# Kernel optimization log

Hardware: AMD Instinct MI355X
Metric: run time of the kernel (lower is better)

## Reference

```python
import jax, jax.numpy as jnp
import numpy as np

B, NQ, NKV, D = 2, 2048, 4096, 1024
H, DH = 16, 64            # qk_channels = v_channels = 1024 -> 16 heads x 64
HID = 2 * int(4.0 * D)    # GEGLU produces 8192 -> split into 2x4096
EPS = 1e-6


def layernorm(x, scale, bias):
    mu = jnp.mean(x, axis=-1, keepdims=True)
    var = jnp.mean(jnp.square(x - mu), axis=-1, keepdims=True)
    return (x - mu) * jax.lax.rsqrt(var + EPS) * scale + bias


def setup_inputs() -> dict:
    key = jax.random.key(0)
    ks = jax.random.split(key, 12)
    s = 0.02
    return {
        "inputs_q": jax.random.normal(ks[0], (B, NQ, D), jnp.float32),
        "inputs_kv": jax.random.normal(ks[1], (B, NKV, D), jnp.float32),
        "ln_q_scale": jnp.ones((D,), jnp.float32),
        "ln_q_bias": jnp.zeros((D,), jnp.float32),
        "ln_kv_scale": jnp.ones((D,), jnp.float32),
        "ln_kv_bias": jnp.zeros((D,), jnp.float32),
        "Wq": s * jax.random.normal(ks[2], (D, H, DH), jnp.float32),
        "bq": jnp.zeros((H, DH), jnp.float32),
        "Wk": s * jax.random.normal(ks[3], (D, H, DH), jnp.float32),
        "bk": jnp.zeros((H, DH), jnp.float32),
        "Wv": s * jax.random.normal(ks[4], (D, H, DH), jnp.float32),
        "bv": jnp.zeros((H, DH), jnp.float32),
        "Wo": s * jax.random.normal(ks[5], (H, DH, D), jnp.float32),
        "bo": jnp.zeros((D,), jnp.float32),
        "ln2_scale": jnp.ones((D,), jnp.float32),
        "ln2_bias": jnp.zeros((D,), jnp.float32),
        "W1": s * jax.random.normal(ks[6], (D, HID), jnp.float32),
        "b1": jnp.zeros((HID,), jnp.float32),
        "W2": s * jax.random.normal(ks[7], (HID // 2, D), jnp.float32),
        "b2": jnp.zeros((D,), jnp.float32),
    }


def reference(inputs_q, inputs_kv, ln_q_scale, ln_q_bias, ln_kv_scale, ln_kv_bias,
              Wq, bq, Wk, bk, Wv, bv, Wo, bo, ln2_scale, ln2_bias, W1, b1, W2, b2):
    ln_q = layernorm(inputs_q, ln_q_scale, ln_q_bias)
    ln_kv = layernorm(inputs_kv, ln_kv_scale, ln_kv_bias)
    # multi-head projections: DenseGeneral to (H, DH)
    q = jnp.einsum('bqd,dhe->bqhe', ln_q, Wq) + bq
    k = jnp.einsum('bkd,dhe->bkhe', ln_kv, Wk) + bk
    v = jnp.einsum('bkd,dhe->bkhe', ln_kv, Wv) + bv
    # scaled dot-product attention (full score matrix, as in source)
    attn = jnp.einsum('bqhd,bkhd->bhqk', q, k) / np.sqrt(DH).astype(np.float32)
    attn = jax.nn.softmax(attn, axis=-1)
    o = jnp.einsum('bhqk,bkhd->bqhd', attn, v)
    # output projection contracting (H, DH)
    x = jnp.einsum('bqhd,hdo->bqo', o, Wo) + bo
    x = x + inputs_q  # query residual
    # GEGLU MLP
    h = layernorm(x, ln2_scale, ln2_bias)
    h = jnp.dot(h, W1) + b1
    a, g = jnp.split(h, 2, axis=-1)
    h = a * jax.nn.gelu(g)  # approximate (tanh) gelu, flax default
    y = jnp.dot(h, W2) + b2
    return x + y
```

## Files before the change

kernel.cpp:

```cpp
#include <hip/hip_runtime.h>

typedef unsigned short u16;
typedef unsigned int u32;
typedef float f32x4 __attribute__((ext_vector_type(4)));
typedef float f32x16 __attribute__((ext_vector_type(16)));
typedef __bf16 bf16x8 __attribute__((ext_vector_type(8)));
typedef short s16x8 __attribute__((ext_vector_type(8)));
typedef short s16x4 __attribute__((ext_vector_type(4)));
typedef u32 u32x4 __attribute__((ext_vector_type(4)));

#define MFMA16(a, b, c) __builtin_amdgcn_mfma_f32_16x16x32_bf16((a), (b), (c), 0, 0, 0)
#define MFMA32(a, b, c) __builtin_amdgcn_mfma_f32_32x32x16_bf16((a), (b), (c), 0, 0, 0)

typedef const __attribute__((address_space(1))) void* gas1_t;
typedef __attribute__((address_space(3))) void* las3_t;
#define GLDS16(g, l) __builtin_amdgcn_global_load_lds((gas1_t)(g), (las3_t)(l), 16, 0, 0)

static __device__ __forceinline__ u16 f2bf(float f) {
  u32 u = __builtin_bit_cast(u32, f);
  u += 0x7FFFu + ((u >> 16) & 1u);
  return (u16)(u >> 16);
}
static __device__ __forceinline__ float bf2f(u16 h) {
  return __builtin_bit_cast(float, (u32)h << 16);
}
static __device__ __forceinline__ u32 cvtpk(float lo, float hi) {
  u32 r;
  asm("v_cvt_pk_bf16_f32 %0, %1, %2" : "=v"(r) : "v"(lo), "v"(hi));
  return r;
}

__global__ __launch_bounds__(256) void transp_cvt(const float* __restrict__ in,
                                                  u16* __restrict__ out, int K, int N,
                                                  float scale) {
  __shared__ u16 t[64][72];
  int k0 = blockIdx.x * 64, n0 = blockIdx.y * 64;
#pragma unroll
  for (int i = 0; i < 16; ++i) {
    int idx = threadIdx.x + i * 256;
    int r = idx >> 6, c = idx & 63;
    t[r][c] = f2bf(in[(size_t)(k0 + r) * N + n0 + c] * scale);
  }
  __syncthreads();
#pragma unroll
  for (int i = 0; i < 16; ++i) {
    int idx = threadIdx.x + i * 256;
    int r = idx >> 6, c = idx & 63;
    out[(size_t)(n0 + r) * K + k0 + c] = t[c][r];
  }
}

__global__ __launch_bounds__(256) void ln_bf16(const float* __restrict__ x,
                                               const float* __restrict__ sc,
                                               const float* __restrict__ bi,
                                               u16* __restrict__ out) {
  int row = blockIdx.x;
  int tid = threadIdx.x;
  float4 v = ((const float4*)(x + (size_t)row * 1024))[tid];
  float s = v.x + v.y + v.z + v.w;
  float s2 = v.x * v.x + v.y * v.y + v.z * v.z + v.w * v.w;
  for (int m = 1; m < 64; m <<= 1) {
    s += __shfl_xor(s, m);
    s2 += __shfl_xor(s2, m);
  }
  __shared__ float rs[4], rs2[4];
  int wave = tid >> 6, lane = tid & 63;
  if (lane == 0) { rs[wave] = s; rs2[wave] = s2; }
  __syncthreads();
  s = rs[0] + rs[1] + rs[2] + rs[3];
  s2 = rs2[0] + rs2[1] + rs2[2] + rs2[3];
  float mu = s * (1.0f / 1024.0f);
  float var = s2 * (1.0f / 1024.0f) - mu * mu;
  float inv = rsqrtf(var + 1e-6f);
  float4 scv = ((const float4*)sc)[tid];
  float4 biv = ((const float4*)bi)[tid];
  s16x4 o;
  o[0] = (short)f2bf((v.x - mu) * inv * scv.x + biv.x);
  o[1] = (short)f2bf((v.y - mu) * inv * scv.y + biv.y);
  o[2] = (short)f2bf((v.z - mu) * inv * scv.z + biv.z);
  o[3] = (short)f2bf((v.w - mu) * inv * scv.w + biv.w);
  *(s16x4*)(out + (size_t)row * 1024 + tid * 4) = o;
}

template <int MODE>
__global__ __launch_bounds__(256) void gemm_nt(const u16* __restrict__ A,
                                               const u16* __restrict__ Bt,
                                               const float* __restrict__ bias,
                                               const float* __restrict__ resid,
                                               void* __restrict__ Cout,
                                               int M, int N, int K, float bias_scale) {
  __shared__ u16 As[128 * 64];
  __shared__ u16 Bs[128 * 64];
  const int m0 = blockIdx.x * 128, n0 = blockIdx.y * 128;
  const int tid = threadIdx.x;
  const int lane = tid & 63, wave = tid >> 6;
  const int wm = (wave >> 1) * 64, wn = (wave & 1) * 64;
  const int lr = lane & 15, hi4 = lane >> 4;
  f32x4 acc[4][4] = {};
  for (int k0 = 0; k0 < K; k0 += 64) {
#pragma unroll
    for (int i = 0; i < 4; ++i) {
      int s = i * 256 + tid;
      int r = s >> 3, slot = s & 7;
      int gslot = slot ^ (r & 7);
      int ldst = (i * 256 + wave * 64) * 8;
      GLDS16(A + (size_t)(m0 + r) * K + k0 + gslot * 8, &As[ldst]);
      GLDS16(Bt + (size_t)(n0 + r) * K + k0 + gslot * 8, &Bs[ldst]);
    }
    __syncthreads();
#pragma unroll
    for (int ks = 0; ks < 2; ++ks) {
      const int sl = ((ks * 4 + hi4) ^ (lr & 7)) * 8;
      bf16x8 af[4], bfr[4];
#pragma unroll
      for (int t = 0; t < 4; ++t) {
        af[t] = __builtin_bit_cast(bf16x8, *(const s16x8*)&As[(wm + t * 16 + lr) * 64 + sl]);
        bfr[t] = __builtin_bit_cast(bf16x8, *(const s16x8*)&Bs[(wn + t * 16 + lr) * 64 + sl]);
      }
#pragma unroll
      for (int mt = 0; mt < 4; ++mt)
#pragma unroll
        for (int nt = 0; nt < 4; ++nt)
          acc[mt][nt] = MFMA16(af[mt], bfr[nt], acc[mt][nt]);
    }
    __syncthreads();
  }
#pragma unroll
  for (int mt = 0; mt < 4; ++mt) {
#pragma unroll
    for (int nt = 0; nt < 4; ++nt) {
      const int ncol = n0 + wn + nt * 16 + lr;
      const float bv = bias[ncol] * bias_scale;
      const int mbase = m0 + wm + mt * 16 + hi4 * 4;
#pragma unroll
      for (int r = 0; r < 4; ++r) {
        const int m = mbase + r;
        const float val = acc[mt][nt][r] + bv;
        if constexpr (MODE == 0) {
          ((u16*)Cout)[(size_t)m * N + ncol] = f2bf(val);
        } else if constexpr (MODE == 1) {
          size_t vidx = ((size_t)((m >> 12) * 1024 + ncol) << 12) | (size_t)(m & 4095);
          ((u16*)Cout)[vidx] = f2bf(val);
        } else {
          ((float*)Cout)[(size_t)m * N + ncol] = val + resid[(size_t)m * N + ncol];
        }
      }
    }
  }
}

__global__ __launch_bounds__(256, 2) void flash_attn(const u16* __restrict__ Qg,
                                                     const u16* __restrict__ Kg,
                                                     const u16* __restrict__ Vt,
                                                     u16* __restrict__ Og) {
  __shared__ u16 Ks[2][64 * 64];
  __shared__ u16 Vs[2][64 * 64];
  const int id = blockIdx.x;
  const int bh = (id & 7) * 4 + ((id >> 3) & 3);
  const int qb = id >> 5;
  const int b = bh >> 4, h = bh & 15;
  const int q0 = qb * 128;
  const int tid = threadIdx.x;
  const int lane = tid & 63, wave = tid >> 6;
  const int lq = lane & 31, hi = lane >> 5;
  const u16* Kbase = Kg + (size_t)(b * 4096) * 1024 + h * 64;
  const u16* Vbase = Vt + (size_t)((b * 16 + h) * 64) * 4096;
  bf16x8 qf[4];
  const size_t qrow = (size_t)(b * 2048 + q0 + wave * 32 + lq);
#pragma unroll
  for (int dc = 0; dc < 4; ++dc)
    qf[dc] = __builtin_bit_cast(bf16x8, *(const s16x8*)&Qg[qrow * 1024 + h * 64 + dc * 16 + hi * 8]);

  f32x16 oacc0 = {}, oacc1 = {};
  float lrun = 0.0f;

  auto stage = [&](int buf, int tile) {
    const int kv0 = tile * 64;
#pragma unroll
    for (int i = 0; i < 2; ++i) {
      int s = i * 256 + tid;
      int r = s >> 3;
      int inb = ((s & 7) * 16) ^ ((r & 7) << 4);
      GLDS16(Kbase + (size_t)(kv0 + r) * 1024 + (inb >> 1), &Ks[buf][(i * 256 + wave * 64) * 8]);
    }
#pragma unroll
    for (int i = 0; i < 2; ++i) {
      int s = i * 256 + tid;
      int r = s >> 3;
      int inb = ((s & 7) * 16) ^ ((r & 7) << 4);
      GLDS16(Vbase + (size_t)r * 4096 + kv0 + (inb >> 1), &Vs[buf][(i * 256 + wave * 64) * 8]);
    }
  };

  stage(0, 0);
  __syncthreads();
  int cur = 0;
  for (int t = 0; t < 64; ++t) {
    if (t < 63) stage(cur ^ 1, t + 1);
    f32x16 sA = {}, sB = {};
#pragma unroll
    for (int dc = 0; dc < 4; ++dc) {
      int row = lq;
      int inb = (dc * 32 + hi * 16) ^ ((row & 7) << 4);
      bf16x8 kf = __builtin_bit_cast(bf16x8, *(const s16x8*)&Ks[cur][row * 64 + (inb >> 1)]);
      sA = MFMA32(kf, qf[dc], sA);
    }
#pragma unroll
    for (int dc = 0; dc < 4; ++dc) {
      int row = 32 + lq;
      int inb = (dc * 32 + hi * 16) ^ ((row & 7) << 4);
      bf16x8 kf = __builtin_bit_cast(bf16x8, *(const s16x8*)&Ks[cur][row * 64 + (inb >> 1)]);
      sB = MFMA32(kf, qf[dc], sB);
    }
    float ts = 0.0f;
#pragma unroll
    for (int i = 0; i < 16; ++i) {
      float p = __builtin_amdgcn_exp2f(sA[i]);
      sA[i] = p;
      ts += p;
    }
#pragma unroll
    for (int i = 0; i < 16; ++i) {
      float p = __builtin_amdgcn_exp2f(sB[i]);
      sB[i] = p;
      ts += p;
    }
    ts += __shfl_xor(ts, 32);
    lrun += ts;
    u32 wa[8], wb[8];
#pragma unroll
    for (int i = 0; i < 8; ++i) wa[i] = cvtpk(sA[2 * i], sA[2 * i + 1]);
#pragma unroll
    for (int i = 0; i < 8; ++i) wb[i] = cvtpk(sB[2 * i], sB[2 * i + 1]);
    u32 a0 = wa[0], c0 = wa[2];
    asm("v_permlane32_swap_b32 %0, %1" : "+v"(a0), "+v"(c0));
    u32 a1 = wa[1], c1 = wa[3];
    asm("v_permlane32_swap_b32 %0, %1" : "+v"(a1), "+v"(c1));
    u32 a2 = wa[4], c2 = wa[6];
    asm("v_permlane32_swap_b32 %0, %1" : "+v"(a2), "+v"(c2));
    u32 a3 = wa[5], c3 = wa[7];
    asm("v_permlane32_swap_b32 %0, %1" : "+v"(a3), "+v"(c3));
    u32 e0 = wb[0], g0 = wb[2];
    asm("v_permlane32_swap_b32 %0, %1" : "+v"(e0), "+v"(g0));
    u32 e1 = wb[1], g1 = wb[3];
    asm("v_permlane32_swap_b32 %0, %1" : "+v"(e1), "+v"(g1));
    u32 e2 = wb[4], g2 = wb[6];
    asm("v_permlane32_swap_b32 %0, %1" : "+v"(e2), "+v"(g2));
    u32 e3 = wb[5], g3 = wb[7];
    asm("v_permlane32_swap_b32 %0, %1" : "+v"(e3), "+v"(g3));
    u32x4 t00 = {a0, a1, c0, c1};
    u32x4 t01 = {a2, a3, c2, c3};
    u32x4 t10 = {e0, e1, g0, g1};
    u32x4 t11 = {e2, e3, g2, g3};
    bf16x8 p00 = __builtin_bit_cast(bf16x8, t00);
    bf16x8 p01 = __builtin_bit_cast(bf16x8, t01);
    bf16x8 p10 = __builtin_bit_cast(bf16x8, t10);
    bf16x8 p11 = __builtin_bit_cast(bf16x8, t11);
#pragma unroll
    for (int st = 0; st < 2; ++st) {
      bf16x8 pc0 = st ? p10 : p00;
      bf16x8 pc1 = st ? p11 : p01;
#pragma unroll
      for (int c = 0; c < 2; ++c) {
        bf16x8 pf = c ? pc1 : pc0;
        {
          int row = lq;
          int inb = (st * 64 + c * 32 + hi * 16) ^ ((row & 7) << 4);
          bf16x8 vf = __builtin_bit_cast(bf16x8, *(const s16x8*)&Vs[cur][row * 64 + (inb >> 1)]);
          oacc0 = MFMA32(vf, pf, oacc0);
        }
        {
          int row = 32 + lq;
          int inb = (st * 64 + c * 32 + hi * 16) ^ ((row & 7) << 4);
          bf16x8 vf = __builtin_bit_cast(bf16x8, *(const s16x8*)&Vs[cur][row * 64 + (inb >> 1)]);
          oacc1 = MFMA32(vf, pf, oacc1);
        }
      }
    }
    __syncthreads();
    cur ^= 1;
  }
  float rinv = 1.0f / lrun;
  u16* obase = Og + qrow * 1024 + h * 64;
#pragma unroll
  for (int rp = 0; rp < 8; ++rp) {
    int r0 = rp * 2;
    int d0 = (r0 & 3) + 8 * (r0 >> 2) + 4 * hi;
    *(u32*)&obase[d0] = cvtpk(oacc0[r0] * rinv, oacc0[r0 + 1] * rinv);
    *(u32*)&obase[32 + d0] = cvtpk(oacc1[r0] * rinv, oacc1[r0 + 1] * rinv);
  }
}

__global__ __launch_bounds__(256) void geglu_k(const u16* __restrict__ h,
                                               u16* __restrict__ out) {
  size_t v = (size_t)blockIdx.x * 256 + threadIdx.x;
  size_t row = v >> 9, c8 = (v & 511) * 8;
  const u16* pa = h + row * 8192 + c8;
  s16x8 va = *(const s16x8*)pa;
  s16x8 vg = *(const s16x8*)(pa + 4096);
  s16x8 o;
#pragma unroll
  for (int j = 0; j < 8; ++j) {
    float a = bf2f((u16)va[j]);
    float gv = bf2f((u16)vg[j]);
    float u = 0.7978845608f * (gv + 0.044715f * gv * gv * gv);
    float e = __expf(2.0f * u);
    float t = 1.0f - 2.0f / (e + 1.0f);
    o[j] = (short)f2bf(a * 0.5f * gv * (1.0f + t));
  }
  *(s16x8*)(out + row * 4096 + c8) = o;
}

extern "C" void kernel_launch(void* const* d_in, const int* in_sizes, int n_in,
                              void* d_out, int out_size, void* d_ws, size_t ws_size,
                              hipStream_t stream) {
  (void)in_sizes; (void)n_in; (void)out_size; (void)ws_size;
  const float* inputs_q = (const float*)d_in[0];
  const float* inputs_kv = (const float*)d_in[1];
  const float* ln_q_scale = (const float*)d_in[2];
  const float* ln_q_bias = (const float*)d_in[3];
  const float* ln_kv_scale = (const float*)d_in[4];
  const float* ln_kv_bias = (const float*)d_in[5];
  const float* Wq = (const float*)d_in[6];
  const float* bq = (const float*)d_in[7];
  const float* Wk = (const float*)d_in[8];
  const float* bk = (const float*)d_in[9];
  const float* Wv = (const float*)d_in[10];
  const float* bv = (const float*)d_in[11];
  const float* Wo = (const float*)d_in[12];
  const float* bo = (const float*)d_in[13];
  const float* ln2_scale = (const float*)d_in[14];
  const float* ln2_bias = (const float*)d_in[15];
  const float* W1 = (const float*)d_in[16];
  const float* b1 = (const float*)d_in[17];
  const float* W2 = (const float*)d_in[18];
  const float* b2 = (const float*)d_in[19];
  float* out = (float*)d_out;
  char* ws = (char*)d_ws;
  const size_t MB = 1ull << 20;
  u16* lnq = (u16*)(ws + 0);
  u16* lnkv = (u16*)(ws + 8 * MB);
  u16* Qb = (u16*)(ws + 24 * MB);
  u16* Kb = (u16*)(ws + 32 * MB);
  u16* Vtb = (u16*)(ws + 48 * MB);
  u16* hfull = (u16*)(ws + 0);
  u16* Ob = (u16*)(ws + 64 * MB);
  float* xbuf = (float*)(ws + 72 * MB);
  u16* ln2b = (u16*)(ws + 88 * MB);
  u16* gg = (u16*)(ws + 96 * MB);
  u16* wqt = (u16*)(ws + 128 * MB);
  u16* wkt = (u16*)(ws + 130 * MB);
  u16* wvt = (u16*)(ws + 132 * MB);
  u16* wot = (u16*)(ws + 134 * MB);
  u16* w1t = (u16*)(ws + 136 * MB);
  u16* w2t = (u16*)(ws + 152 * MB);

  const float QSC = 0.125f * 1.44269504088896f;
  dim3 blk(256);
  transp_cvt<<<dim3(16, 16), blk, 0, stream>>>(Wq, wqt, 1024, 1024, QSC);
  transp_cvt<<<dim3(16, 16), blk, 0, stream>>>(Wk, wkt, 1024, 1024, 1.0f);
  transp_cvt<<<dim3(16, 16), blk, 0, stream>>>(Wv, wvt, 1024, 1024, 1.0f);
  transp_cvt<<<dim3(16, 16), blk, 0, stream>>>(Wo, wot, 1024, 1024, 1.0f);
  transp_cvt<<<dim3(16, 128), blk, 0, stream>>>(W1, w1t, 1024, 8192, 1.0f);
  transp_cvt<<<dim3(64, 16), blk, 0, stream>>>(W2, w2t, 4096, 1024, 1.0f);
  ln_bf16<<<4096, blk, 0, stream>>>(inputs_q, ln_q_scale, ln_q_bias, lnq);
  ln_bf16<<<8192, blk, 0, stream>>>(inputs_kv, ln_kv_scale, ln_kv_bias, lnkv);
  gemm_nt<0><<<dim3(32, 8), blk, 0, stream>>>(lnq, wqt, bq, nullptr, Qb, 4096, 1024, 1024, QSC);
  gemm_nt<0><<<dim3(64, 8), blk, 0, stream>>>(lnkv, wkt, bk, nullptr, Kb, 8192, 1024, 1024, 1.0f);
  gemm_nt<1><<<dim3(64, 8), blk, 0, stream>>>(lnkv, wvt, bv, nullptr, Vtb, 8192, 1024, 1024, 1.0f);
  flash_attn<<<dim3(512), blk, 0, stream>>>(Qb, Kb, Vtb, Ob);
  gemm_nt<2><<<dim3(32, 8), blk, 0, stream>>>(Ob, wot, bo, inputs_q, xbuf, 4096, 1024, 1024, 1.0f);
  ln_bf16<<<4096, blk, 0, stream>>>(xbuf, ln2_scale, ln2_bias, ln2b);
  gemm_nt<0><<<dim3(32, 64), blk, 0, stream>>>(ln2b, w1t, b1, nullptr, hfull, 4096, 8192, 1024, 1.0f);
  geglu_k<<<8192, blk, 0, stream>>>(hfull, gg);
  gemm_nt<2><<<dim3(32, 8), blk, 0, stream>>>(gg, w2t, b2, xbuf, out, 4096, 1024, 4096, 1.0f);
}
```

Baseline: 409.8 us.

## Fuse GEGLU into W1 GEMM epilogue, remap workgroups, tune attention priorities

W1 is reordered at conversion time so each 32-column group holds 16 'a' columns followed by their 16 matching gate columns. This lets the W1 GEMM epilogue apply GELU gating directly and write the 4096-wide bf16 output, so the separate GEGLU kernel and the 8192-wide intermediate round trip go away. The GEMM also remaps workgroup IDs in blocks of 8 (an XCD-aware swizzle) to improve cache locality across dies. In the attention kernel, MFMA sections are wrapped in s_setprio and the row-sum is reduced as a tree instead of a serial chain.

```diff
diff --git a/kernel.cpp b/kernel.cpp
--- a/kernel.cpp
+++ b/kernel.cpp
@@ -29,6 +29,12 @@
   asm("v_cvt_pk_bf16_f32 %0, %1, %2" : "=v"(r) : "v"(lo), "v"(hi));
   return r;
 }
+static __device__ __forceinline__ float gelu_t(float g) {
+  float u = 0.7978845608f * (g + 0.044715f * g * g * g);
+  float e = __expf(2.0f * u);
+  float t = 1.0f - 2.0f / (e + 1.0f);
+  return 0.5f * g * (1.0f + t);
+}
 
 __global__ __launch_bounds__(256) void transp_cvt(const float* __restrict__ in,
                                                   u16* __restrict__ out, int K, int N,
@@ -47,6 +53,27 @@
     int idx = threadIdx.x + i * 256;
     int r = idx >> 6, c = idx & 63;
     out[(size_t)(n0 + r) * K + k0 + c] = t[c][r];
+  }
+}
+
+__global__ __launch_bounds__(256) void geglu_transp(const float* __restrict__ in,
+                                                    u16* __restrict__ out) {
+  __shared__ u16 t[64][72];
+  int k0 = blockIdx.x * 64, n0 = blockIdx.y * 64;
+#pragma unroll
+  for (int i = 0; i < 16; ++i) {
+    int idx = threadIdx.x + i * 256;
+    int r = idx >> 6, c = idx & 63;
+    int np = n0 + c;
+    int orig = ((np >> 5) << 4) + (np & 15) + (((np >> 4) & 1) << 12);
+    t[r][c] = f2bf(in[(size_t)(k0 + r) * 8192 + orig]);
+  }
+  __syncthreads();
+#pragma unroll
+  for (int i = 0; i < 16; ++i) {
+    int idx = threadIdx.x + i * 256;
+    int r = idx >> 6, c = idx & 63;
+    out[(size_t)(n0 + r) * 1024 + k0 + c] = t[c][r];
   }
 }
 
@@ -91,7 +118,11 @@
                                                int M, int N, int K, float bias_scale) {
   __shared__ u16 As[128 * 64];
   __shared__ u16 Bs[128 * 64];
-  const int m0 = blockIdx.x * 128, n0 = blockIdx.y * 128;
+  const int nbx = gridDim.x;
+  const int nwg = nbx * gridDim.y;
+  const int wg0 = blockIdx.y * nbx + blockIdx.x;
+  const int wg = (nwg & 7) ? wg0 : (wg0 & 7) * (nwg >> 3) + (wg0 >> 3);
+  const int m0 = (wg % nbx) * 128, n0 = (wg / nbx) * 128;
   const int tid = threadIdx.x;
   const int lane = tid & 63, wave = tid >> 6;
   const int wm = (wave >> 1) * 64, wn = (wave & 1) * 64;
@@ -125,24 +156,44 @@
     }
     __syncthreads();
   }
-#pragma unroll
-  for (int mt = 0; mt < 4; ++mt) {
-#pragma unroll
-    for (int nt = 0; nt < 4; ++nt) {
-      const int ncol = n0 + wn + nt * 16 + lr;
-      const float bv = bias[ncol] * bias_scale;
+  if constexpr (MODE == 3) {
+#pragma unroll
+    for (int mt = 0; mt < 4; ++mt) {
       const int mbase = m0 + wm + mt * 16 + hi4 * 4;
 #pragma unroll
-      for (int r = 0; r < 4; ++r) {
-        const int m = mbase + r;
-        const float val = acc[mt][nt][r] + bv;
-        if constexpr (MODE == 0) {
-          ((u16*)Cout)[(size_t)m * N + ncol] = f2bf(val);
-        } else if constexpr (MODE == 1) {
-          size_t vidx = ((size_t)((m >> 12) * 1024 + ncol) << 12) | (size_t)(m & 4095);
-          ((u16*)Cout)[vidx] = f2bf(val);
-        } else {
-          ((float*)Cout)[(size_t)m * N + ncol] = val + resid[(size_t)m * N + ncol];
+      for (int p = 0; p < 2; ++p) {
+        const int oc = (((n0 + wn + p * 32) >> 5) << 4) + lr;
+        const float ba = bias[oc];
+        const float bg = bias[oc + 4096];
+#pragma unroll
+        for (int r = 0; r < 4; ++r) {
+          const int m = mbase + r;
+          float a = acc[mt][2 * p][r] + ba;
+          float g = acc[mt][2 * p + 1][r] + bg;
+          ((u16*)Cout)[(size_t)m * 4096 + oc] = f2bf(a * gelu_t(g));
+        }
+      }
+    }
+  } else {
+#pragma unroll
+    for (int mt = 0; mt < 4; ++mt) {
+#pragma unroll
+      for (int nt = 0; nt < 4; ++nt) {
+        const int ncol = n0 + wn + nt * 16 + lr;
+        const float bv = bias[ncol] * bias_scale;
+        const int mbase = m0 + wm + mt * 16 + hi4 * 4;
+#pragma unroll
+        for (int r = 0; r < 4; ++r) {
+          const int m = mbase + r;
+          const float val = acc[mt][nt][r] + bv;
+          if constexpr (MODE == 0) {
+            ((u16*)Cout)[(size_t)m * N + ncol] = f2bf(val);
+          } else if constexpr (MODE == 1) {
+            size_t vidx = ((size_t)((m >> 12) * 1024 + ncol) << 12) | (size_t)(m & 4095);
+            ((u16*)Cout)[vidx] = f2bf(val);
+          } else {
+            ((float*)Cout)[(size_t)m * N + ncol] = val + resid[(size_t)m * N + ncol];
+          }
         }
       }
     }
@@ -198,6 +249,7 @@
   for (int t = 0; t < 64; ++t) {
     if (t < 63) stage(cur ^ 1, t + 1);
     f32x16 sA = {}, sB = {};
+    __builtin_amdgcn_s_setprio(1);
 #pragma unroll
     for (int dc = 0; dc < 4; ++dc) {
       int row = lq;
@@ -212,19 +264,20 @@
       bf16x8 kf = __builtin_bit_cast(bf16x8, *(const s16x8*)&Ks[cur][row * 64 + (inb >> 1)]);
       sB = MFMA32(kf, qf[dc], sB);
     }
-    float ts = 0.0f;
-#pragma unroll
-    for (int i = 0; i < 16; ++i) {
-      float p = __builtin_amdgcn_exp2f(sA[i]);
-      sA[i] = p;
-      ts += p;
-    }
-#pragma unroll
-    for (int i = 0; i < 16; ++i) {
-      float p = __builtin_amdgcn_exp2f(sB[i]);
-      sB[i] = p;
-      ts += p;
-    }
+    __builtin_amdgcn_s_setprio(0);
+#pragma unroll
+    for (int i = 0; i < 16; ++i) sA[i] = __builtin_amdgcn_exp2f(sA[i]);
+#pragma unroll
+    for (int i = 0; i < 16; ++i) sB[i] = __builtin_amdgcn_exp2f(sB[i]);
+    float a0 = (sA[0] + sA[1]) + (sA[2] + sA[3]);
+    float a1 = (sA[4] + sA[5]) + (sA[6] + sA[7]);
+    float a2 = (sA[8] + sA[9]) + (sA[10] + sA[11]);
+    float a3 = (sA[12] + sA[13]) + (sA[14] + sA[15]);
+    float b0 = (sB[0] + sB[1]) + (sB[2] + sB[3]);
+    float b1s = (sB[4] + sB[5]) + (sB[6] + sB[7]);
+    float b2s = (sB[8] + sB[9]) + (sB[10] + sB[11]);
+    float b3 = (sB[12] + sB[13]) + (sB[14] + sB[15]);
+    float ts = ((a0 + a1) + (a2 + a3)) + ((b0 + b1s) + (b2s + b3));
     ts += __shfl_xor(ts, 32);
     lrun += ts;
     u32 wa[8], wb[8];
@@ -232,14 +285,14 @@
     for (int i = 0; i < 8; ++i) wa[i] = cvtpk(sA[2 * i], sA[2 * i + 1]);
 #pragma unroll
     for (int i = 0; i < 8; ++i) wb[i] = cvtpk(sB[2 * i], sB[2 * i + 1]);
-    u32 a0 = wa[0], c0 = wa[2];
-    asm("v_permlane32_swap_b32 %0, %1" : "+v"(a0), "+v"(c0));
-    u32 a1 = wa[1], c1 = wa[3];
-    asm("v_permlane32_swap_b32 %0, %1" : "+v"(a1), "+v"(c1));
-    u32 a2 = wa[4], c2 = wa[6];
-    asm("v_permlane32_swap_b32 %0, %1" : "+v"(a2), "+v"(c2));
-    u32 a3 = wa[5], c3 = wa[7];
-    asm("v_permlane32_swap_b32 %0, %1" : "+v"(a3), "+v"(c3));
+    u32 a0w = wa[0], c0 = wa[2];
+    asm("v_permlane32_swap_b32 %0, %1" : "+v"(a0w), "+v"(c0));
+    u32 a1w = wa[1], c1 = wa[3];
+    asm("v_permlane32_swap_b32 %0, %1" : "+v"(a1w), "+v"(c1));
+    u32 a2w = wa[4], c2 = wa[6];
+    asm("v_permlane32_swap_b32 %0, %1" : "+v"(a2w), "+v"(c2));
+    u32 a3w = wa[5], c3 = wa[7];
+    asm("v_permlane32_swap_b32 %0, %1" : "+v"(a3w), "+v"(c3));
     u32 e0 = wb[0], g0 = wb[2];
     asm("v_permlane32_swap_b32 %0, %1" : "+v"(e0), "+v"(g0));
     u32 e1 = wb[1], g1 = wb[3];
@@ -248,14 +301,15 @@
     asm("v_permlane32_swap_b32 %0, %1" : "+v"(e2), "+v"(g2));
     u32 e3 = wb[5], g3 = wb[7];
     asm("v_permlane32_swap_b32 %0, %1" : "+v"(e3), "+v"(g3));
-    u32x4 t00 = {a0, a1, c0, c1};
-    u32x4 t01 = {a2, a3, c2, c3};
+    u32x4 t00 = {a0w, a1w, c0, c1};
+    u32x4 t01 = {a2w, a3w, c2, c3};
     u32x4 t10 = {e0, e1, g0, g1};
     u32x4 t11 = {e2, e3, g2, g3};
     bf16x8 p00 = __builtin_bit_cast(bf16x8, t00);
     bf16x8 p01 = __builtin_bit_cast(bf16x8, t01);
     bf16x8 p10 = __builtin_bit_cast(bf16x8, t10);
     bf16x8 p11 = __builtin_bit_cast(bf16x8, t11);
+    __builtin_amdgcn_s_setprio(1);
 #pragma unroll
     for (int st = 0; st < 2; ++st) {
       bf16x8 pc0 = st ? p10 : p00;
@@ -277,6 +331,7 @@
         }
       }
     }
+    __builtin_amdgcn_s_setprio(0);
     __syncthreads();
     cur ^= 1;
   }
@@ -289,26 +344,6 @@
     *(u32*)&obase[d0] = cvtpk(oacc0[r0] * rinv, oacc0[r0 + 1] * rinv);
     *(u32*)&obase[32 + d0] = cvtpk(oacc1[r0] * rinv, oacc1[r0 + 1] * rinv);
   }
-}
-
-__global__ __launch_bounds__(256) void geglu_k(const u16* __restrict__ h,
-                                               u16* __restrict__ out) {
-  size_t v = (size_t)blockIdx.x * 256 + threadIdx.x;
-  size_t row = v >> 9, c8 = (v & 511) * 8;
-  const u16* pa = h + row * 8192 + c8;
-  s16x8 va = *(const s16x8*)pa;
-  s16x8 vg = *(const s16x8*)(pa + 4096);
-  s16x8 o;
-#pragma unroll
-  for (int j = 0; j < 8; ++j) {
-    float a = bf2f((u16)va[j]);
-    float gv = bf2f((u16)vg[j]);
-    float u = 0.7978845608f * (gv + 0.044715f * gv * gv * gv);
-    float e = __expf(2.0f * u);
-    float t = 1.0f - 2.0f / (e + 1.0f);
-    o[j] = (short)f2bf(a * 0.5f * gv * (1.0f + t));
-  }
-  *(s16x8*)(out + row * 4096 + c8) = o;
 }
 
 extern "C" void kernel_launch(void* const* d_in, const int* in_sizes, int n_in,
@@ -343,7 +378,6 @@
   u16* Qb = (u16*)(ws + 24 * MB);
   u16* Kb = (u16*)(ws + 32 * MB);
   u16* Vtb = (u16*)(ws + 48 * MB);
-  u16* hfull = (u16*)(ws + 0);
   u16* Ob = (u16*)(ws + 64 * MB);
   float* xbuf = (float*)(ws + 72 * MB);
   u16* ln2b = (u16*)(ws + 88 * MB);
@@ -352,7 +386,7 @@
   u16* wkt = (u16*)(ws + 130 * MB);
   u16* wvt = (u16*)(ws + 132 * MB);
   u16* wot = (u16*)(ws + 134 * MB);
-  u16* w1t = (u16*)(ws + 136 * MB);
+  u16* w1i = (u16*)(ws + 136 * MB);
   u16* w2t = (u16*)(ws + 152 * MB);
 
   const float QSC = 0.125f * 1.44269504088896f;
@@ -361,7 +395,7 @@
   transp_cvt<<<dim3(16, 16), blk, 0, stream>>>(Wk, wkt, 1024, 1024, 1.0f);
   transp_cvt<<<dim3(16, 16), blk, 0, stream>>>(Wv, wvt, 1024, 1024, 1.0f);
   transp_cvt<<<dim3(16, 16), blk, 0, stream>>>(Wo, wot, 1024, 1024, 1.0f);
-  transp_cvt<<<dim3(16, 128), blk, 0, stream>>>(W1, w1t, 1024, 8192, 1.0f);
+  geglu_transp<<<dim3(16, 128), blk, 0, stream>>>(W1, w1i);
   transp_cvt<<<dim3(64, 16), blk, 0, stream>>>(W2, w2t, 4096, 1024, 1.0f);
   ln_bf16<<<4096, blk, 0, stream>>>(inputs_q, ln_q_scale, ln_q_bias, lnq);
   ln_bf16<<<8192, blk, 0, stream>>>(inputs_kv, ln_kv_scale, ln_kv_bias, lnkv);
@@ -371,7 +405,6 @@
   flash_attn<<<dim3(512), blk, 0, stream>>>(Qb, Kb, Vtb, Ob);
   gemm_nt<2><<<dim3(32, 8), blk, 0, stream>>>(Ob, wot, bo, inputs_q, xbuf, 4096, 1024, 1024, 1.0f);
   ln_bf16<<<4096, blk, 0, stream>>>(xbuf, ln2_scale, ln2_bias, ln2b);
-  gemm_nt<0><<<dim3(32, 64), blk, 0, stream>>>(ln2b, w1t, b1, nullptr, hfull, 4096, 8192, 1024, 1.0f);
-  geglu_k<<<8192, blk, 0, stream>>>(hfull, gg);
+  gemm_nt<3><<<dim3(32, 64), blk, 0, stream>>>(ln2b, w1i, b1, nullptr, gg, 4096, 8192, 1024, 1.0f);
   gemm_nt<2><<<dim3(32, 8), blk, 0, stream>>>(gg, w2t, b2, xbuf, out, 4096, 1024, 4096, 1.0f);
 }
```

After: 410.5 us. Within noise of the previous version (+0.2%).
